# Optimization experiments

Hardware: AMD Instinct MI355X
Metric: run time of the kernel (lower is better)

Reference implementation:

```python
import jax, jax.numpy as jnp
import numpy as np

N, NODE_DIM, EDGE_DIM, E, H, L, G = 100000, 128, 16, 1200000, 64, 3, 1000


def gcn_conv(x, w, b, row, col, dis):
    # PyG GCNConv: x @ W, symmetric-normalized aggregation with self-loops, + bias
    xw = x @ w                                    # [N, H]
    norm = dis[row] * dis[col]                    # [E]
    msg = norm[:, None] * xw[row]                 # [E, H]
    out = jax.ops.segment_sum(msg, col, num_segments=N)
    out = out + (dis * dis)[:, None] * xw         # self-loop contribution
    return out + b


def reference(x, edge_attr, node_w, node_b, edge_w, edge_b, conv_w, conv_b,
              cls_w1, cls_b1, cls_w2, cls_b2, edge_index, batch, num_graphs):
    row, col = edge_index[0], edge_index[1]
    # node embed
    h = x @ node_w + node_b                       # [N, H]
    # edge embed aggregated to both endpoints
    e = edge_attr @ edge_w + edge_b               # [E, H]
    edge_aggr = jax.ops.segment_sum(e, row, num_segments=N) \
              + jax.ops.segment_sum(e, col, num_segments=N)
    h = h + edge_aggr
    # degree with self-loops (deg over col, matching PyG GCNConv default flow)
    deg = jax.ops.segment_sum(jnp.ones((E,), h.dtype), col, num_segments=N) + 1.0
    dis = jnp.where(deg > 0, jax.lax.rsqrt(deg), 0.0)
    xs = []
    for i in range(L):
        h = jax.nn.relu(gcn_conv(h, conv_w[i], conv_b[i], row, col, dis))
        xs.append(h)
    hj = jnp.concatenate(xs, axis=-1)             # JumpingKnowledge 'cat' -> [N, L*H]
    # global mean pool over batch index
    sums = jax.ops.segment_sum(hj, batch, num_segments=num_graphs)
    cnts = jax.ops.segment_sum(jnp.ones((N,), hj.dtype), batch, num_segments=num_graphs)
    pooled = sums / jnp.maximum(cnts, 1.0)[:, None]  # [G, L*H]
    # classifier (eval mode: dropout is identity)
    z = jax.nn.relu(pooled @ cls_w1 + cls_b1)
    out = z @ cls_w2 + cls_b2                     # [G, 1]
    return out.squeeze(-1)


def setup_inputs() -> dict:
    key = jax.random.key(0)
    ks = jax.random.split(key, 16)
    s = lambda fan: 1.0 / np.sqrt(fan)
    return {
        "x": jax.random.normal(ks[0], (N, NODE_DIM), jnp.float32),
        "edge_attr": jax.random.normal(ks[1], (E, EDGE_DIM), jnp.float32),
        "node_w": jax.random.uniform(ks[2], (NODE_DIM, H), jnp.float32, -s(NODE_DIM), s(NODE_DIM)),
        "node_b": jnp.zeros((H,), jnp.float32),
        "edge_w": jax.random.uniform(ks[3], (EDGE_DIM, H), jnp.float32, -s(EDGE_DIM), s(EDGE_DIM)),
        "edge_b": jnp.zeros((H,), jnp.float32),
        "conv_w": jax.random.uniform(ks[4], (L, H, H), jnp.float32, -s(H), s(H)),
        "conv_b": jnp.zeros((L, H), jnp.float32),
        "cls_w1": jax.random.uniform(ks[5], (L * H, H // 2), jnp.float32, -s(L * H), s(L * H)),
        "cls_b1": jnp.zeros((H // 2,), jnp.float32),
        "cls_w2": jax.random.uniform(ks[6], (H // 2, 1), jnp.float32, -s(H // 2), s(H // 2)),
        "cls_b2": jnp.zeros((1,), jnp.float32),
        "edge_index": jax.random.randint(ks[7], (2, E), 0, N, jnp.int64 if jax.config.jax_enable_x64 else jnp.int32),
        "batch": jnp.sort(jax.random.randint(ks[8], (N,), 0, G, jnp.int64 if jax.config.jax_enable_x64 else jnp.int32)),
        "num_graphs": G,
    }
```

## Files before the change

kernel.cpp:

```cpp
#include <hip/hip_runtime.h>
#include <math.h>


#define EPB 4096

__global__ __launch_bounds__(256) void k_embed(
    const float* __restrict__ x, const float* __restrict__ w,
    const float* __restrict__ b, float* __restrict__ out, int N) {
  __shared__ __align__(16) float rl[64 * 128];
  const int t = threadIdx.x;
  const int j = t & 63;
  const int wv = t >> 6;
  const int base = blockIdx.x * 64;
  float wr[128];
#pragma unroll
  for (int k = 0; k < 128; ++k) wr[k] = w[k * 64 + j];
  const float bj = b[j];
#pragma unroll
  for (int it = 0; it < 8; ++it) {
    int lin = (t + it * 256) * 4;
    int r = lin >> 7, c = lin & 127;
    int row = base + r;
    float4 v = (row < N) ? *(const float4*)&x[(size_t)row * 128 + c]
                         : make_float4(0.f, 0.f, 0.f, 0.f);
    *(float4*)&rl[lin] = v;
  }
  __syncthreads();
  for (int r = wv; r < 64; r += 4) {
    int row = base + r;
    if (row >= N) break;
    float acc = bj;
#pragma unroll
    for (int k4 = 0; k4 < 32; ++k4) {
      float4 a = *(const float4*)&rl[r * 128 + k4 * 4];
      acc = fmaf(a.x, wr[k4 * 4 + 0], acc);
      acc = fmaf(a.y, wr[k4 * 4 + 1], acc);
      acc = fmaf(a.z, wr[k4 * 4 + 2], acc);
      acc = fmaf(a.w, wr[k4 * 4 + 3], acc);
    }
    out[(size_t)row * 64 + j] = acc;
  }
}

__global__ __launch_bounds__(256) void k_conv(
    const float* __restrict__ hin, const float* __restrict__ w,
    const float* __restrict__ dis, float* __restrict__ xws, int N) {
  __shared__ __align__(16) float rl[64 * 64];
  const int t = threadIdx.x;
  const int j = t & 63;
  const int wv = t >> 6;
  const int base = blockIdx.x * 64;
  float wr[64];
#pragma unroll
  for (int k = 0; k < 64; ++k) wr[k] = w[k * 64 + j];
#pragma unroll
  for (int it = 0; it < 4; ++it) {
    int lin = (t + it * 256) * 4;
    int r = lin >> 6, c = lin & 63;
    int row = base + r;
    float4 v = (row < N) ? *(const float4*)&hin[(size_t)row * 64 + c]
                         : make_float4(0.f, 0.f, 0.f, 0.f);
    *(float4*)&rl[lin] = v;
  }
  __syncthreads();
  for (int r = wv; r < 64; r += 4) {
    int row = base + r;
    if (row >= N) break;
    float acc = 0.f;
#pragma unroll
    for (int k4 = 0; k4 < 16; ++k4) {
      float4 a = *(const float4*)&rl[r * 64 + k4 * 4];
      acc = fmaf(a.x, wr[k4 * 4 + 0], acc);
      acc = fmaf(a.y, wr[k4 * 4 + 1], acc);
      acc = fmaf(a.z, wr[k4 * 4 + 2], acc);
      acc = fmaf(a.w, wr[k4 * 4 + 3], acc);
    }
    xws[(size_t)row * 64 + j] = dis[row] * acc;
  }
}

__global__ __launch_bounds__(256) void k_hist(
    const int* __restrict__ erow, const int* __restrict__ ecol,
    int* __restrict__ matTc, int* __restrict__ matTr, int E, int NB, int NBLK) {
  __shared__ int hc[512], hr[512];
  int b = blockIdx.x, t = threadIdx.x;
  for (int i = t; i < NB; i += 256) { hc[i] = 0; hr[i] = 0; }
  __syncthreads();
  int e0 = b * EPB;
#pragma unroll
  for (int q = 0; q < 16; ++q) {
    int e = e0 + q * 256 + t;
    if (e < E) {
      atomicAdd(&hc[ecol[e] >> 8], 1);
      atomicAdd(&hr[erow[e] >> 8], 1);
    }
  }
  __syncthreads();
  for (int i = t; i < NB; i += 256) {
    matTc[(size_t)i * NBLK + b] = hc[i];
    matTr[(size_t)i * NBLK + b] = hr[i];
  }
}

__global__ __launch_bounds__(256) void kBscan(
    int* __restrict__ matT, int* __restrict__ tot, int NBLK) {
  __shared__ int sc[256];
  int i = blockIdx.x, t = threadIdx.x;
  int* row = matT + (size_t)i * NBLK;
  int e0 = (2 * t < NBLK) ? row[2 * t] : 0;
  int e1 = (2 * t + 1 < NBLK) ? row[2 * t + 1] : 0;
  int s = e0 + e1;
  sc[t] = s;
  __syncthreads();
  for (int d = 1; d < 256; d <<= 1) {
    int x = (t >= d) ? sc[t - d] : 0;
    __syncthreads();
    sc[t] += x;
    __syncthreads();
  }
  int excl = sc[t] - s;
  if (2 * t < NBLK) row[2 * t] = excl;
  if (2 * t + 1 < NBLK) row[2 * t + 1] = excl + e0;
  if (t == 255) tot[i] = sc[255];
}

__global__ __launch_bounds__(512) void kB2(
    const int* __restrict__ tot, int* __restrict__ start, int NB) {
  __shared__ int sc[512];
  int t = threadIdx.x;
  int s = (t < NB) ? tot[t] : 0;
  sc[t] = s;
  __syncthreads();
  for (int d = 1; d < 512; d <<= 1) {
    int x = (t >= d) ? sc[t - d] : 0;
    __syncthreads();
    sc[t] += x;
    __syncthreads();
  }
  if (t < NB) start[t] = sc[t] - s;
}

__global__ __launch_bounds__(256) void k_scat(
    const int* __restrict__ erow, const int* __restrict__ ecol,
    const int* __restrict__ matTc, const int* __restrict__ matTr,
    const int* __restrict__ startc, const int* __restrict__ startr,
    unsigned long long* __restrict__ tmpc, unsigned int* __restrict__ tmpr,
    int E, int NB, int NBLK) {
  __shared__ int curc[512], curr[512];
  int b = blockIdx.x, t = threadIdx.x;
  for (int i = t; i < NB; i += 256) {
    curc[i] = startc[i] + matTc[(size_t)i * NBLK + b];
    curr[i] = startr[i] + matTr[(size_t)i * NBLK + b];
  }
  __syncthreads();
  int e0 = b * EPB;
#pragma unroll
  for (int q = 0; q < 16; ++q) {
    int e = e0 + q * 256 + t;
    if (e < E) {
      int r = erow[e], c = ecol[e];
      int pc = atomicAdd(&curc[c >> 8], 1);
      tmpc[pc] = (unsigned long long)(c & 255) |
                 ((unsigned long long)r << 8) |
                 ((unsigned long long)e << 25);
      int pr = atomicAdd(&curr[r >> 8], 1);
      tmpr[pr] = ((unsigned int)e << 8) | (unsigned int)(r & 255);
    }
  }
}

__global__ __launch_bounds__(256) void k_bcount_c(
    const unsigned long long* __restrict__ tmpc, const int* __restrict__ startc,
    const int* __restrict__ totc, int* __restrict__ indeg,
    int* __restrict__ offc, int N) {
  __shared__ int h[256], sc[256];
  int b = blockIdx.x, t = threadIdx.x;
  h[t] = 0;
  __syncthreads();
  int bstart = startc[b], cnt = totc[b];
  for (int i = t; i < cnt; i += 256)
    atomicAdd(&h[(int)(tmpc[bstart + i] & 255)], 1);
  __syncthreads();
  int s = h[t];
  sc[t] = s;
  __syncthreads();
  for (int d = 1; d < 256; d <<= 1) {
    int x = (t >= d) ? sc[t - d] : 0;
    __syncthreads();
    sc[t] += x;
    __syncthreads();
  }
  int n = (b << 8) + t;
  if (n < N) {
    indeg[n] = s;
    offc[n] = bstart + sc[t] - s;
  }
}

__global__ __launch_bounds__(256) void k_bcount_r(
    const unsigned int* __restrict__ tmpr, const int* __restrict__ startr,
    const int* __restrict__ totr, int* __restrict__ outdeg,
    int* __restrict__ offr, int N) {
  __shared__ int h[256], sc[256];
  int b = blockIdx.x, t = threadIdx.x;
  h[t] = 0;
  __syncthreads();
  int bstart = startr[b], cnt = totr[b];
  for (int i = t; i < cnt; i += 256)
    atomicAdd(&h[(int)(tmpr[bstart + i] & 255)], 1);
  __syncthreads();
  int s = h[t];
  sc[t] = s;
  __syncthreads();
  for (int d = 1; d < 256; d <<= 1) {
    int x = (t >= d) ? sc[t - d] : 0;
    __syncthreads();
    sc[t] += x;
    __syncthreads();
  }
  int n = (b << 8) + t;
  if (n < N) {
    outdeg[n] = s;
    offr[n] = bstart + sc[t] - s;
  }
}

__global__ __launch_bounds__(256) void k_place_c(
    const unsigned long long* __restrict__ tmpc, const int* __restrict__ offc,
    int2* __restrict__ lst2, int N, int E) {
  __shared__ int cur[256];
  int b = blockIdx.x, t = threadIdx.x;
  int colbase = b << 8;
  int nb = min(256, N - colbase);
  if (t < nb) cur[t] = offc[colbase + t];
  __syncthreads();
  int bstart = offc[colbase];
  int bend = (colbase + 256 < N) ? offc[colbase + 256] : E;
  for (int idx = bstart + t; idx < bend; idx += 256) {
    unsigned long long v = tmpc[idx];
    int lc = (int)(v & 255);
    int src = (int)((v >> 8) & 0x1FFFF);
    int eid = (int)(v >> 25);
    int p = atomicAdd(&cur[lc], 1);
    int2 w; w.x = src; w.y = eid;
    lst2[p] = w;
  }
}

__global__ __launch_bounds__(256) void k_place_r(
    const unsigned int* __restrict__ tmpr, const int* __restrict__ offr,
    int* __restrict__ eidr, int N, int E) {
  __shared__ int cur[256];
  int b = blockIdx.x, t = threadIdx.x;
  int rowbase = b << 8;
  int nb = min(256, N - rowbase);
  if (t < nb) cur[t] = offr[rowbase + t];
  __syncthreads();
  int bstart = offr[rowbase];
  int bend = (rowbase + 256 < N) ? offr[rowbase + 256] : E;
  for (int idx = bstart + t; idx < bend; idx += 256) {
    unsigned int v = tmpr[idx];
    int lr = (int)(v & 255);
    int p = atomicAdd(&cur[lr], 1);
    eidr[p] = (int)(v >> 8);
  }
}

__global__ __launch_bounds__(256) void k_eembed(
    const float* __restrict__ ea, const int2* __restrict__ lst2,
    const int* __restrict__ eidr, const int* __restrict__ offc,
    const int* __restrict__ indeg, const int* __restrict__ offr,
    const int* __restrict__ outdeg, const float* __restrict__ ew,
    const float* __restrict__ eb, float* h0, float* __restrict__ dis, int N) {
  int t = blockIdx.x * 256 + threadIdx.x;
  int n = __builtin_amdgcn_readfirstlane(t >> 6);
  if (n >= N) return;
  int lane = threadIdx.x & 63;
  int slot = lane >> 4, kk = lane & 15;
  int cin = indeg[n], basec = offc[n];
  int cout = outdeg[n], baser = offr[n];
  float acc = 0.f;
  int c0 = (cin > 0) ? cin - 1 : 0;
  for (int i = 0; i < cin; i += 16) {
#pragma unroll
    for (int q = 0; q < 4; ++q) {
      int idx = i + q * 4 + slot;
      int eid = lst2[basec + min(idx, c0)].y;
      float v = ea[(size_t)eid * 16 + kk];
      acc += (idx < cin) ? v : 0.f;
    }
  }
  int r0 = (cout > 0) ? cout - 1 : 0;
  for (int i = 0; i < cout; i += 16) {
#pragma unroll
    for (int q = 0; q < 4; ++q) {
      int idx = i + q * 4 + slot;
      int eid = eidr[baser + min(idx, r0)];
      float v = ea[(size_t)eid * 16 + kk];
      acc += (idx < cout) ? v : 0.f;
    }
  }
  acc += __shfl_xor(acc, 16, 64);
  acc += __shfl_xor(acc, 32, 64);
  int j = lane;
  float v = h0[(size_t)n * 64 + j] + (float)(cin + cout) * eb[j];
#pragma unroll
  for (int k = 0; k < 16; ++k) {
    float ak = __shfl(acc, k, 64);
    v = fmaf(ak, ew[k * 64 + j], v);
  }
  h0[(size_t)n * 64 + j] = v;
  if (j == 0) dis[n] = 1.0f / sqrtf((float)cin + 1.0f);
}

__global__ __launch_bounds__(256) void k_gather(
    const float* __restrict__ xws, const float* __restrict__ dis,
    const int* __restrict__ offc, const int* __restrict__ indeg,
    const int2* __restrict__ lst2, const float* __restrict__ b,
    float* __restrict__ h0, float* __restrict__ hj_slice, int N) {
  int t = blockIdx.x * 256 + threadIdx.x;
  int j = t & 63;
  int n = __builtin_amdgcn_readfirstlane(t >> 6);
  if (n >= N) return;
  int cnt = indeg[n];
  int base = offc[n];
  int c0 = (cnt > 0) ? cnt - 1 : 0;
  float acc = xws[(size_t)n * 64 + j];
  for (int i = 0; i < cnt; i += 16) {
    float s[16];
#pragma unroll
    for (int q = 0; q < 16; ++q) {
      int src = lst2[base + min(i + q, c0)].x;
      s[q] = xws[(size_t)src * 64 + j];
    }
#pragma unroll
    for (int q = 0; q < 16; ++q)
      acc += (i + q < cnt) ? s[q] : 0.f;
  }
  float act = fmaxf(fmaf(dis[n], acc, b[j]), 0.f);
  h0[(size_t)n * 64 + j] = act;
  hj_slice[(size_t)n * 192 + j] = act;
}

__global__ __launch_bounds__(192) void k_pool(
    const float* __restrict__ hj, const int* __restrict__ batch, int N,
    const float* __restrict__ w1, const float* __restrict__ b1,
    const float* __restrict__ w2, const float* __restrict__ b2,
    float* __restrict__ out) {
  __shared__ float pl[192];
  int g = blockIdx.x;
  int t = threadIdx.x;
  int lo = 0, hi = N;
  while (lo < hi) { int m = (lo + hi) >> 1; if (batch[m] < g) lo = m + 1; else hi = m; }
  int start = lo;
  hi = N;
  while (lo < hi) { int m = (lo + hi) >> 1; if (batch[m] < g + 1) lo = m + 1; else hi = m; }
  int end = lo;
  float s = 0.f;
  for (int r = start; r < end; ++r) s += hj[(size_t)r * 192 + t];
  int cnt = end - start;
  pl[t] = s / (float)(cnt > 0 ? cnt : 1);
  __syncthreads();
  if (t < 64) {
    float val = 0.f;
    if (t < 32) {
      float z = b1[t];
#pragma unroll 8
      for (int k = 0; k < 192; ++k) z = fmaf(pl[k], w1[k * 32 + t], z);
      z = fmaxf(z, 0.f);
      val = z * w2[t];
    }
#pragma unroll
    for (int off = 16; off > 0; off >>= 1) val += __shfl_down(val, off);
    if (t == 0) out[g] = val + b2[0];
  }
}

extern "C" void kernel_launch(void* const* d_in, const int* in_sizes, int n_in,
                              void* d_out, int out_size, void* d_ws, size_t ws_size,
                              hipStream_t stream) {
  const float* x      = (const float*)d_in[0];
  const float* ea     = (const float*)d_in[1];
  const float* node_w = (const float*)d_in[2];
  const float* node_b = (const float*)d_in[3];
  const float* edge_w = (const float*)d_in[4];
  const float* edge_b = (const float*)d_in[5];
  const float* conv_w = (const float*)d_in[6];
  const float* conv_b = (const float*)d_in[7];
  const float* w1     = (const float*)d_in[8];
  const float* b1     = (const float*)d_in[9];
  const float* w2     = (const float*)d_in[10];
  const float* b2     = (const float*)d_in[11];
  const int*   ei     = (const int*)d_in[12];
  const int*   batch  = (const int*)d_in[13];

  const int N = in_sizes[0] / 128;
  const int E = in_sizes[12] / 2;
  const int G = out_size;
  const int* erow = ei;
  const int* ecol = ei + E;

  float* ws = (float*)d_ws;
  size_t o = 0;
  float* h0    = ws + o; o += (size_t)N * 64;
  float* xws   = ws + o; o += (size_t)N * 64;
  float* hj    = ws + o; o += (size_t)N * 192;
  float* dis   = ws + o; o += N;
  int* indeg   = (int*)(ws + o); o += N;
  int* outdeg  = (int*)(ws + o); o += N;
  int* offc    = (int*)(ws + o); o += N;
  int* offr    = (int*)(ws + o); o += N;
  int2* lst2   = (int2*)(ws + o); o += (size_t)2 * E;

  const int NB = (N + 255) >> 8;
  const int NBLK = (E + EPB - 1) / EPB;
  unsigned long long* tmpc = (unsigned long long*)hj;
  unsigned int* tmpr = (unsigned int*)(hj + (size_t)2 * E);
  int* eidr  = (int*)(hj + (size_t)3 * E);
  int* matTc = (int*)(hj + (size_t)4 * E);
  int* matTr = matTc + (size_t)NB * NBLK;
  int* totc  = matTr + (size_t)NB * NBLK;
  int* startc = totc + NB;
  int* totr  = startc + NB;
  int* startr = totr + NB;
  float* out = (float*)d_out;

  dim3 b256(256);

  k_embed<<<(N + 63) / 64, b256, 0, stream>>>(x, node_w, node_b, h0, N);
  k_hist<<<NBLK, b256, 0, stream>>>(erow, ecol, matTc, matTr, E, NB, NBLK);
  kBscan<<<NB, b256, 0, stream>>>(matTc, totc, NBLK);
  kBscan<<<NB, b256, 0, stream>>>(matTr, totr, NBLK);
  kB2<<<1, dim3(512), 0, stream>>>(totc, startc, NB);
  kB2<<<1, dim3(512), 0, stream>>>(totr, startr, NB);
  k_scat<<<NBLK, b256, 0, stream>>>(erow, ecol, matTc, matTr, startc, startr,
                                    tmpc, tmpr, E, NB, NBLK);
  k_bcount_c<<<NB, b256, 0, stream>>>(tmpc, startc, totc, indeg, offc, N);
  k_bcount_r<<<NB, b256, 0, stream>>>(tmpr, startr, totr, outdeg, offr, N);
  k_place_c<<<NB, b256, 0, stream>>>(tmpc, offc, lst2, N, E);
  k_place_r<<<NB, b256, 0, stream>>>(tmpr, offr, eidr, N, E);
  k_eembed<<<((size_t)N * 64 + 255) / 256, b256, 0, stream>>>(
      ea, lst2, eidr, offc, indeg, offr, outdeg, edge_w, edge_b, h0, dis, N);
  for (int l = 0; l < 3; ++l) {
    k_conv<<<(N + 63) / 64, b256, 0, stream>>>(
        h0, conv_w + (size_t)l * 64 * 64, dis, xws, N);
    k_gather<<<((size_t)N * 64 + 255) / 256, b256, 0, stream>>>(
        xws, dis, offc, indeg, lst2, conv_b + (size_t)l * 64,
        h0, hj + (size_t)l * 64, N);
  }
  k_pool<<<G, dim3(192), 0, stream>>>(hj, batch, N, w1, b1, w2, b2, out);
}
```

Before: 473.0 us.

## Merge CSR build kernels, split edge lists, vectorize neighbor gather

Merges the paired column/row scan, count and place kernels into single launches with twice the blocks, which cuts launch count. Splits the interleaved int2 (src, eid) list into separate src and eid arrays so each consumer reads only the field it needs. Rewrites the per-layer neighbor gather to process four nodes per wavefront with float4 loads and eight-way unrolling. It also skips the h0 write on the last layer and widens the edge-embed unroll. The risk is lower occupancy from the larger float4 register arrays and some extra branching in the merged kernels.

```diff
diff --git a/kernel.cpp b/kernel.cpp
--- a/kernel.cpp
+++ b/kernel.cpp
@@ -103,10 +103,14 @@
 }
 
 __global__ __launch_bounds__(256) void kBscan(
-    int* __restrict__ matT, int* __restrict__ tot, int NBLK) {
+    int* __restrict__ matTc, int* __restrict__ matTr,
+    int* __restrict__ totc, int* __restrict__ totr, int NB, int NBLK) {
   __shared__ int sc[256];
-  int i = blockIdx.x, t = threadIdx.x;
-  int* row = matT + (size_t)i * NBLK;
+  int bi = blockIdx.x, t = threadIdx.x;
+  int side = (bi >= NB) ? 1 : 0;
+  int i = bi - side * NB;
+  int* row = (side ? matTr : matTc) + (size_t)i * NBLK;
+  int* tot = side ? totr : totc;
   int e0 = (2 * t < NBLK) ? row[2 * t] : 0;
   int e1 = (2 * t + 1 < NBLK) ? row[2 * t + 1] : 0;
   int s = e0 + e1;
@@ -125,9 +129,12 @@
 }
 
 __global__ __launch_bounds__(512) void kB2(
-    const int* __restrict__ tot, int* __restrict__ start, int NB) {
+    const int* __restrict__ totc, const int* __restrict__ totr,
+    int* __restrict__ startc, int* __restrict__ startr, int NB) {
   __shared__ int sc[512];
   int t = threadIdx.x;
+  const int* tot = blockIdx.x ? totr : totc;
+  int* start = blockIdx.x ? startr : startc;
   int s = (t < NB) ? tot[t] : 0;
   sc[t] = s;
   __syncthreads();
@@ -169,17 +176,28 @@
   }
 }
 
-__global__ __launch_bounds__(256) void k_bcount_c(
-    const unsigned long long* __restrict__ tmpc, const int* __restrict__ startc,
-    const int* __restrict__ totc, int* __restrict__ indeg,
-    int* __restrict__ offc, int N) {
+__global__ __launch_bounds__(256) void k_bcount(
+    const unsigned long long* __restrict__ tmpc,
+    const unsigned int* __restrict__ tmpr,
+    const int* __restrict__ startc, const int* __restrict__ startr,
+    const int* __restrict__ totc, const int* __restrict__ totr,
+    int* __restrict__ indeg, int* __restrict__ outdeg,
+    int* __restrict__ offc, int* __restrict__ offr, int N, int NB) {
   __shared__ int h[256], sc[256];
-  int b = blockIdx.x, t = threadIdx.x;
+  int bi = blockIdx.x, t = threadIdx.x;
+  int side = (bi >= NB) ? 1 : 0;
+  int b = bi - side * NB;
   h[t] = 0;
   __syncthreads();
-  int bstart = startc[b], cnt = totc[b];
-  for (int i = t; i < cnt; i += 256)
-    atomicAdd(&h[(int)(tmpc[bstart + i] & 255)], 1);
+  int bstart = side ? startr[b] : startc[b];
+  int cnt = side ? totr[b] : totc[b];
+  if (side) {
+    for (int i = t; i < cnt; i += 256)
+      atomicAdd(&h[(int)(tmpr[bstart + i] & 255)], 1);
+  } else {
+    for (int i = t; i < cnt; i += 256)
+      atomicAdd(&h[(int)(tmpc[bstart + i] & 255)], 1);
+  }
   __syncthreads();
   int s = h[t];
   sc[t] = s;
@@ -192,82 +210,46 @@
   }
   int n = (b << 8) + t;
   if (n < N) {
-    indeg[n] = s;
-    offc[n] = bstart + sc[t] - s;
-  }
-}
-
-__global__ __launch_bounds__(256) void k_bcount_r(
-    const unsigned int* __restrict__ tmpr, const int* __restrict__ startr,
-    const int* __restrict__ totr, int* __restrict__ outdeg,
-    int* __restrict__ offr, int N) {
-  __shared__ int h[256], sc[256];
-  int b = blockIdx.x, t = threadIdx.x;
-  h[t] = 0;
-  __syncthreads();
-  int bstart = startr[b], cnt = totr[b];
-  for (int i = t; i < cnt; i += 256)
-    atomicAdd(&h[(int)(tmpr[bstart + i] & 255)], 1);
-  __syncthreads();
-  int s = h[t];
-  sc[t] = s;
-  __syncthreads();
-  for (int d = 1; d < 256; d <<= 1) {
-    int x = (t >= d) ? sc[t - d] : 0;
-    __syncthreads();
-    sc[t] += x;
-    __syncthreads();
-  }
-  int n = (b << 8) + t;
-  if (n < N) {
-    outdeg[n] = s;
-    offr[n] = bstart + sc[t] - s;
-  }
-}
-
-__global__ __launch_bounds__(256) void k_place_c(
-    const unsigned long long* __restrict__ tmpc, const int* __restrict__ offc,
-    int2* __restrict__ lst2, int N, int E) {
+    if (side) { outdeg[n] = s; offr[n] = bstart + sc[t] - s; }
+    else      { indeg[n] = s;  offc[n] = bstart + sc[t] - s; }
+  }
+}
+
+__global__ __launch_bounds__(256) void k_place(
+    const unsigned long long* __restrict__ tmpc,
+    const unsigned int* __restrict__ tmpr,
+    const int* __restrict__ offc, const int* __restrict__ offr,
+    int* __restrict__ srcl, int* __restrict__ eidc, int* __restrict__ eidr,
+    int N, int E, int NB) {
   __shared__ int cur[256];
-  int b = blockIdx.x, t = threadIdx.x;
-  int colbase = b << 8;
-  int nb = min(256, N - colbase);
-  if (t < nb) cur[t] = offc[colbase + t];
-  __syncthreads();
-  int bstart = offc[colbase];
-  int bend = (colbase + 256 < N) ? offc[colbase + 256] : E;
-  for (int idx = bstart + t; idx < bend; idx += 256) {
-    unsigned long long v = tmpc[idx];
-    int lc = (int)(v & 255);
-    int src = (int)((v >> 8) & 0x1FFFF);
-    int eid = (int)(v >> 25);
-    int p = atomicAdd(&cur[lc], 1);
-    int2 w; w.x = src; w.y = eid;
-    lst2[p] = w;
-  }
-}
-
-__global__ __launch_bounds__(256) void k_place_r(
-    const unsigned int* __restrict__ tmpr, const int* __restrict__ offr,
-    int* __restrict__ eidr, int N, int E) {
-  __shared__ int cur[256];
-  int b = blockIdx.x, t = threadIdx.x;
-  int rowbase = b << 8;
-  int nb = min(256, N - rowbase);
-  if (t < nb) cur[t] = offr[rowbase + t];
-  __syncthreads();
-  int bstart = offr[rowbase];
-  int bend = (rowbase + 256 < N) ? offr[rowbase + 256] : E;
-  for (int idx = bstart + t; idx < bend; idx += 256) {
-    unsigned int v = tmpr[idx];
-    int lr = (int)(v & 255);
-    int p = atomicAdd(&cur[lr], 1);
-    eidr[p] = (int)(v >> 8);
+  int bi = blockIdx.x, t = threadIdx.x;
+  int side = (bi >= NB) ? 1 : 0;
+  int b = bi - side * NB;
+  const int* off = side ? offr : offc;
+  int nodebase = b << 8;
+  int nb = min(256, N - nodebase);
+  if (t < nb) cur[t] = off[nodebase + t];
+  __syncthreads();
+  int bstart = off[nodebase];
+  int bend = (nodebase + 256 < N) ? off[nodebase + 256] : E;
+  if (side) {
+    for (int idx = bstart + t; idx < bend; idx += 256) {
+      unsigned int v = tmpr[idx];
+      int p = atomicAdd(&cur[(int)(v & 255)], 1);
+      eidr[p] = (int)(v >> 8);
+    }
+  } else {
+    for (int idx = bstart + t; idx < bend; idx += 256) {
+      unsigned long long v = tmpc[idx];
+      int p = atomicAdd(&cur[(int)(v & 255)], 1);
+      srcl[p] = (int)((v >> 8) & 0x1FFFF);
+      eidc[p] = (int)(v >> 25);
+    }
   }
 }
 
 __global__ __launch_bounds__(256) void k_eembed(
-    const float* __restrict__ ea, const int2* __restrict__ lst2,
+    const float* __restrict__ ea, const int* __restrict__ eidc,
     const int* __restrict__ eidr, const int* __restrict__ offc,
     const int* __restrict__ indeg, const int* __restrict__ offr,
     const int* __restrict__ outdeg, const float* __restrict__ ew,
@@ -281,19 +263,19 @@
   int cout = outdeg[n], baser = offr[n];
   float acc = 0.f;
   int c0 = (cin > 0) ? cin - 1 : 0;
-  for (int i = 0; i < cin; i += 16) {
-#pragma unroll
-    for (int q = 0; q < 4; ++q) {
+  for (int i = 0; i < cin; i += 32) {
+#pragma unroll
+    for (int q = 0; q < 8; ++q) {
       int idx = i + q * 4 + slot;
-      int eid = lst2[basec + min(idx, c0)].y;
+      int eid = eidc[basec + min(idx, c0)];
       float v = ea[(size_t)eid * 16 + kk];
       acc += (idx < cin) ? v : 0.f;
     }
   }
   int r0 = (cout > 0) ? cout - 1 : 0;
-  for (int i = 0; i < cout; i += 16) {
-#pragma unroll
-    for (int q = 0; q < 4; ++q) {
+  for (int i = 0; i < cout; i += 32) {
+#pragma unroll
+    for (int q = 0; q < 8; ++q) {
       int idx = i + q * 4 + slot;
       int eid = eidr[baser + min(idx, r0)];
       float v = ea[(size_t)eid * 16 + kk];
@@ -316,30 +298,44 @@
 __global__ __launch_bounds__(256) void k_gather(
     const float* __restrict__ xws, const float* __restrict__ dis,
     const int* __restrict__ offc, const int* __restrict__ indeg,
-    const int2* __restrict__ lst2, const float* __restrict__ b,
+    const int* __restrict__ srcl, const float* __restrict__ b,
     float* __restrict__ h0, float* __restrict__ hj_slice, int N) {
-  int t = blockIdx.x * 256 + threadIdx.x;
-  int j = t & 63;
-  int n = __builtin_amdgcn_readfirstlane(t >> 6);
-  if (n >= N) return;
-  int cnt = indeg[n];
-  int base = offc[n];
+  const int t = threadIdx.x;
+  const int lane = t & 63;
+  const int s = lane >> 4;
+  const int fg = lane & 15;
+  int n = blockIdx.x * 16 + (t >> 6) * 4 + s;
+  bool ok = (n < N);
+  int nn = ok ? n : (N - 1);
+  int cnt = indeg[nn];
+  int boff = offc[nn];
   int c0 = (cnt > 0) ? cnt - 1 : 0;
-  float acc = xws[(size_t)n * 64 + j];
-  for (int i = 0; i < cnt; i += 16) {
-    float s[16];
-#pragma unroll
-    for (int q = 0; q < 16; ++q) {
-      int src = lst2[base + min(i + q, c0)].x;
-      s[q] = xws[(size_t)src * 64 + j];
-    }
-#pragma unroll
-    for (int q = 0; q < 16; ++q)
-      acc += (i + q < cnt) ? s[q] : 0.f;
-  }
-  float act = fmaxf(fmaf(dis[n], acc, b[j]), 0.f);
-  h0[(size_t)n * 64 + j] = act;
-  hj_slice[(size_t)n * 192 + j] = act;
+  float4 acc = *(const float4*)&xws[(size_t)nn * 64 + fg * 4];
+  for (int i = 0; i < cnt; i += 8) {
+    float4 v[8];
+#pragma unroll
+    for (int q = 0; q < 8; ++q) {
+      int src = srcl[boff + min(i + q, c0)];
+      v[q] = *(const float4*)&xws[(size_t)src * 64 + fg * 4];
+    }
+#pragma unroll
+    for (int q = 0; q < 8; ++q) {
+      if (i + q < cnt) {
+        acc.x += v[q].x; acc.y += v[q].y; acc.z += v[q].z; acc.w += v[q].w;
+      }
+    }
+  }
+  float d = dis[nn];
+  float4 bb = *(const float4*)&b[fg * 4];
+  float4 act;
+  act.x = fmaxf(fmaf(d, acc.x, bb.x), 0.f);
+  act.y = fmaxf(fmaf(d, acc.y, bb.y), 0.f);
+  act.z = fmaxf(fmaf(d, acc.z, bb.z), 0.f);
+  act.w = fmaxf(fmaf(d, acc.w, bb.w), 0.f);
+  if (ok) {
+    if (h0 != nullptr) *(float4*)&h0[(size_t)n * 64 + fg * 4] = act;
+    *(float4*)&hj_slice[(size_t)n * 192 + fg * 4] = act;
+  }
 }
 
 __global__ __launch_bounds__(192) void k_pool(
@@ -410,14 +406,15 @@
   int* outdeg  = (int*)(ws + o); o += N;
   int* offc    = (int*)(ws + o); o += N;
   int* offr    = (int*)(ws + o); o += N;
-  int2* lst2   = (int2*)(ws + o); o += (size_t)2 * E;
+  int* srcl    = (int*)(ws + o); o += E;
+  int* eidc    = (int*)(ws + o); o += E;
+  int* eidr    = (int*)(ws + o); o += E;
 
   const int NB = (N + 255) >> 8;
   const int NBLK = (E + EPB - 1) / EPB;
   unsigned long long* tmpc = (unsigned long long*)hj;
   unsigned int* tmpr = (unsigned int*)(hj + (size_t)2 * E);
-  int* eidr  = (int*)(hj + (size_t)3 * E);
-  int* matTc = (int*)(hj + (size_t)4 * E);
+  int* matTc = (int*)(hj + (size_t)3 * E);
   int* matTr = matTc + (size_t)NB * NBLK;
   int* totc  = matTr + (size_t)NB * NBLK;
   int* startc = totc + NB;
@@ -426,27 +423,26 @@
   float* out = (float*)d_out;
 
   dim3 b256(256);
-
-  k_embed<<<(N + 63) / 64, b256, 0, stream>>>(x, node_w, node_b, h0, N);
+  const int NT = (N + 63) / 64;
+
+  k_embed<<<NT, b256, 0, stream>>>(x, node_w, node_b, h0, N);
   k_hist<<<NBLK, b256, 0, stream>>>(erow, ecol, matTc, matTr, E, NB, NBLK);
-  kBscan<<<NB, b256, 0, stream>>>(matTc, totc, NBLK);
-  kBscan<<<NB, b256, 0, stream>>>(matTr, totr, NBLK);
-  kB2<<<1, dim3(512), 0, stream>>>(totc, startc, NB);
-  kB2<<<1, dim3(512), 0, stream>>>(totr, startr, NB);
+  kBscan<<<2 * NB, b256, 0, stream>>>(matTc, matTr, totc, totr, NB, NBLK);
+  kB2<<<2, dim3(512), 0, stream>>>(totc, totr, startc, startr, NB);
   k_scat<<<NBLK, b256, 0, stream>>>(erow, ecol, matTc, matTr, startc, startr,
                                     tmpc, tmpr, E, NB, NBLK);
-  k_bcount_c<<<NB, b256, 0, stream>>>(tmpc, startc, totc, indeg, offc, N);
-  k_bcount_r<<<NB, b256, 0, stream>>>(tmpr, startr, totr, outdeg, offr, N);
-  k_place_c<<<NB, b256, 0, stream>>>(tmpc, offc, lst2, N, E);
-  k_place_r<<<NB, b256, 0, stream>>>(tmpr, offr, eidr, N, E);
+  k_bcount<<<2 * NB, b256, 0, stream>>>(tmpc, tmpr, startc, startr, totc, totr,
+                                        indeg, outdeg, offc, offr, N, NB);
+  k_place<<<2 * NB, b256, 0, stream>>>(tmpc, tmpr, offc, offr,
+                                       srcl, eidc, eidr, N, E, NB);
   k_eembed<<<((size_t)N * 64 + 255) / 256, b256, 0, stream>>>(
-      ea, lst2, eidr, offc, indeg, offr, outdeg, edge_w, edge_b, h0, dis, N);
+      ea, eidc, eidr, offc, indeg, offr, outdeg, edge_w, edge_b, h0, dis, N);
   for (int l = 0; l < 3; ++l) {
-    k_conv<<<(N + 63) / 64, b256, 0, stream>>>(
+    k_conv<<<NT, b256, 0, stream>>>(
         h0, conv_w + (size_t)l * 64 * 64, dis, xws, N);
-    k_gather<<<((size_t)N * 64 + 255) / 256, b256, 0, stream>>>(
-        xws, dis, offc, indeg, lst2, conv_b + (size_t)l * 64,
-        h0, hj + (size_t)l * 64, N);
+    k_gather<<<(N + 15) / 16, b256, 0, stream>>>(
+        xws, dis, offc, indeg, srcl, conv_b + (size_t)l * 64,
+        (l < 2) ? h0 : nullptr, hj + (size_t)l * 64, N);
   }
   k_pool<<<G, dim3(192), 0, stream>>>(hj, batch, N, w1, b1, w2, b2, out);
 }
```

After: 457.3 us. -3.3%, faster.
